# Kernel tuning notes

Measured on AMD Instinct MI355X. Metric: run time of the kernel, lower is better.

The kernel has to match this reference:

```python
import jax, jax.numpy as jnp
import numpy as np

D_MODEL = 640
KW = 32                                  # kernel_width -> content_kernel (compression (1,1))
SUPER = np.array([5, 5, 2, 1, 1])        # supersampling per subhead
DIL = np.array([1, 1, 2, 4, 8])          # dilation rate per subhead
SUBHEADS = 5
HEADS = int(SUPER.sum())                 # 14
DH = D_MODEL // SUBHEADS                 # 128
B, N = 2, 1024
KC = KW                                  # content kernel width
DIL_PER_HEAD = np.repeat(DIL, SUPER)     # dilation used by each of the 14 value heads


def _windows(seq, bias, dil):
    """Banded (dilated, stride-1, 'same'-padded) windows of a projected sequence.

    seq: (B, N, DH). The original zero-pads the raw sequence, then applies the
    per-head Linear; projecting a zero vector yields the bias, so padding the
    projected sequence with `bias` is mathematically identical.
    Returns (B, N, KC, DH) with out[b, l, j] = padded[b, l + j*dil].
    """
    dil = int(dil)
    pad_total = (KC - 1) * dil           # effective kernel minus 1, stride 1 -> same length
    pl = pad_total // 2
    pr = pad_total - pl
    b = seq.shape[0]
    left = jnp.broadcast_to(bias, (b, pl, DH))
    right = jnp.broadcast_to(bias, (b, pr, DH))
    padded = jnp.concatenate([left, seq, right], axis=1)
    idx = jnp.arange(N)[:, None] + jnp.arange(KC)[None, :] * dil  # (N, KC)
    return padded[:, idx]


def setup_inputs() -> dict:
    key = jax.random.key(0)
    ks = jax.random.split(key, 13)
    f = lambda k, sh, s=1.0: jax.random.normal(k, sh, dtype=jnp.float32) * s
    return {
        "query": f(ks[0], (B, N, D_MODEL)),
        "key": f(ks[1], (B, N, D_MODEL)),
        "value": f(ks[2], (B, N, D_MODEL)),
        "Qk": f(ks[3], (SUBHEADS, DH, D_MODEL), 0.04),
        "Qb": f(ks[4], (SUBHEADS, DH), 0.02),
        "Kk": f(ks[5], (SUBHEADS, DH, D_MODEL), 0.04),
        "Kb": f(ks[6], (SUBHEADS, DH), 0.02),
        "Vk": f(ks[7], (HEADS, DH, D_MODEL), 0.04),
        "Vb": f(ks[8], (HEADS, DH), 0.02),
        "Sk": f(ks[9], (HEADS, KC, KC), 0.1),   # Pos_Sampling kernel, Kq=1 so in=out=KC
        "Sb": f(ks[10], (HEADS, KC), 0.02),
        "Ck": f(ks[11], (D_MODEL, HEADS * DH), 0.02),  # Collapse kernel
        "Cb": f(ks[12], (D_MODEL,), 0.0),
    }


def reference(query, key, value, Qk, Qb, Kk, Kb, Vk, Vb, Sk, Sb, Ck, Cb):
    # Per-subhead Q/K projections (query_kernel=1, stride=1 -> one query per position)
    q = jnp.einsum('bnd,sod->bnso', query, Qk) + Qb          # (B,N,5,DH)
    kproj = jnp.einsum('bnd,sod->bnso', key, Kk) + Kb        # (B,N,5,DH)
    kwin = jnp.stack(
        [_windows(kproj[:, :, s], Kb[s], DIL[s]) for s in range(SUBHEADS)],
        axis=2)                                              # (B,N,5,KC,DH)
    # Banded scores (original applies no 1/sqrt(d) scaling)
    score = jnp.einsum('bnsd,bnskd->bnsk', q, kwin)          # (B,N,5,KC)
    # Supersample subhead scores into heads, then learned positional resampling
    score = jnp.repeat(score, SUPER, axis=2, total_repeat_length=HEADS)  # (B,N,14,KC)
    score = jnp.einsum('bnhk,hjk->bnhj', score, Sk) + Sb     # Pos_Sampling Linear
    w = jax.nn.softmax(score, axis=-1)
    # Per-head value projection; each head windows with its subhead's dilation
    vproj = jnp.einsum('bnd,hod->bnho', value, Vk) + Vb      # (B,N,14,DH)
    vwin = jnp.stack(
        [_windows(vproj[:, :, h], Vb[h], DIL_PER_HEAD[h]) for h in range(HEADS)],
        axis=2)                                              # (B,N,14,KC,DH)
    attn = jnp.einsum('bnhk,bnhkd->bnhd', w, vwin)           # (B,N,14,DH)
    flat = attn.reshape(attn.shape[0], attn.shape[1], HEADS * DH)
    return jnp.einsum('bnf,of->bno', flat, Ck) + Cb          # (B,N,D_MODEL)
```

## Files before the change

kernel.cpp:

```cpp
#include <hip/hip_runtime.h>
#include <hip/hip_bf16.h>

using bf16 = __hip_bfloat16;
typedef __attribute__((ext_vector_type(8))) short s16x8;
typedef __attribute__((ext_vector_type(4))) short s16x4;
typedef __attribute__((ext_vector_type(4))) float f32x4;
typedef unsigned int u32;

__device__ __forceinline__ float b2f(short u) {
    union { float f; u32 i; } x; x.i = ((u32)(unsigned short)u) << 16; return x.f;
}
__device__ __forceinline__ short f2b(float f) {
    bf16 h = (bf16)f; return *(short*)&h;
}

__device__ __forceinline__ void g2l16(const void* g, void* l) {
    __builtin_amdgcn_global_load_lds(
        (const __attribute__((address_space(1))) void*)g,
        (__attribute__((address_space(3))) void*)l, 16, 0, 0);
}

struct CvtArgs { const float* src[10]; bf16* dst[10]; int n[10]; int bb[11]; };
__global__ __launch_bounds__(256)
void convert_kernel(CvtArgs a) {
    const int blk = blockIdx.x;
    int s = 0;
    while (s < 9 && blk >= a.bb[s + 1]) ++s;
    const int base = (blk - a.bb[s]) * 1024 + threadIdx.x * 4;
    if (base >= a.n[s]) return;
    float4 v = *(const float4*)(a.src[s] + base);
    ushort4 o;
    o.x = (unsigned short)f2b(v.x); o.y = (unsigned short)f2b(v.y);
    o.z = (unsigned short)f2b(v.z); o.w = (unsigned short)f2b(v.w);
    *(ushort4*)(a.dst[s] + base) = o;
}

template<int BM, int BN, bool A_F32, bool OUT_F32>
__device__ __forceinline__ void gemm_pipe(
    const void* __restrict__ A, const bf16* __restrict__ W,
    const bf16* __restrict__ bias, void* __restrict__ out,
    int m0, int n0, int N, int K, bf16* lA, bf16* lB) {
    constexpr int WM = BM / 2, WN = BN / 2, FM = WM / 16, FN = WN / 16;
    constexpr int SA = BM / 64;
    constexpr int CA = BM / 64;
    constexpr int CB = BN / 64;
    constexpr int ASZ = BM * 32, BSZ = BN * 32;
    const int tid = threadIdx.x;
    const int wave = tid >> 6;
    const int lane = tid & 63;
    const int wr = wave >> 1, wc = wave & 1;
    const int quad = lane >> 4, lm = lane & 15;
    uint4 ra[SA];

    auto issueB = [&](int k0, int buf) {
#pragma unroll
        for (int c = 0; c < CB; ++c) {
            const int sl = c * 256 + tid, row = sl >> 2, col = (sl & 3) * 8;
            g2l16(W + (size_t)(n0 + row) * K + k0 + col,
                  lB + buf * BSZ + (c * 256 + wave * 64) * 8);
        }
    };
    auto issueA = [&](int k0, int buf) {
#pragma unroll
        for (int c = 0; c < CA; ++c) {
            const int sl = c * 256 + tid, row = sl >> 2, col = (sl & 3) * 8;
            g2l16((const bf16*)A + (size_t)(m0 + row) * K + k0 + col,
                  lA + buf * ASZ + (c * 256 + wave * 64) * 8);
        }
    };
    auto loadA_f32 = [&](int k0) {
#pragma unroll
        for (int q = 0; q < SA; ++q) {
            const int sl = q * 256 + tid, row = sl >> 2, col = (sl & 3) * 8;
            const float* g = (const float*)A + (size_t)(m0 + row) * K + k0 + col;
            float4 f0 = *(const float4*)g;
            float4 f1 = *(const float4*)(g + 4);
            union { uint4 u; short h[8]; } p;
            p.h[0] = f2b(f0.x); p.h[1] = f2b(f0.y); p.h[2] = f2b(f0.z); p.h[3] = f2b(f0.w);
            p.h[4] = f2b(f1.x); p.h[5] = f2b(f1.y); p.h[6] = f2b(f1.z); p.h[7] = f2b(f1.w);
            ra[q] = p.u;
        }
    };
    auto writeA = [&](int buf) {
#pragma unroll
        for (int q = 0; q < SA; ++q)
            *(uint4*)(lA + buf * ASZ + (q * 256 + tid) * 8) = ra[q];
    };

    f32x4 acc[FM][FN] = {};
    issueB(0, 0);
    if (A_F32) { loadA_f32(0); writeA(0); } else { issueA(0, 0); }
    __syncthreads();

    int cur = 0;
    for (int k0 = 0; k0 < K; k0 += 32) {
        const bool more = (k0 + 32 < K);
        if (more) {
            issueB(k0 + 32, cur ^ 1);
            if (A_F32) loadA_f32(k0 + 32); else issueA(k0 + 32, cur ^ 1);
        }
        s16x8 af[FM], bf_[FN];
#pragma unroll
        for (int i = 0; i < FM; ++i)
            af[i] = *(const s16x8*)&lA[cur * ASZ + (wr * WM + i * 16 + lm) * 32 + quad * 8];
#pragma unroll
        for (int j = 0; j < FN; ++j)
            bf_[j] = *(const s16x8*)&lB[cur * BSZ + (wc * WN + j * 16 + lm) * 32 + quad * 8];
#pragma unroll
        for (int i = 0; i < FM; ++i)
#pragma unroll
            for (int j = 0; j < FN; ++j)
                acc[i][j] = __builtin_amdgcn_mfma_f32_16x16x32_bf16(af[i], bf_[j], acc[i][j], 0, 0, 0);
        if (more && A_F32) writeA(cur ^ 1);
        __syncthreads();
        cur ^= 1;
    }
#pragma unroll
    for (int i = 0; i < FM; ++i) {
        const int rbase = m0 + wr * WM + i * 16 + quad * 4;
#pragma unroll
        for (int j = 0; j < FN; ++j) {
            const int col = n0 + wc * WN + j * 16 + lm;
            const float bv = (float)bias[col];
#pragma unroll
            for (int r = 0; r < 4; ++r) {
                float v = acc[i][j][r] + bv;
                size_t off = (size_t)(rbase + r) * N + col;
                if (OUT_F32) ((float*)out)[off] = v;
                else         ((bf16*)out)[off] = (bf16)v;
            }
        }
    }
}

__global__ __launch_bounds__(256)
void proj_kernel(const float* __restrict__ q, const float* __restrict__ k,
                 const float* __restrict__ v,
                 const bf16* __restrict__ Qkc, const bf16* __restrict__ Kkc,
                 const bf16* __restrict__ Vkc,
                 const bf16* __restrict__ Qbc, const bf16* __restrict__ Kbc,
                 const bf16* __restrict__ Vbc,
                 bf16* __restrict__ qp, bf16* __restrict__ kp,
                 bf16* __restrict__ vp) {
    __shared__ __align__(16) bf16 lA[2 * 128 * 32];
    __shared__ __align__(16) bf16 lB[2 * 64 * 32];
    const int L = blockIdx.x, xcd = L & 7, i = L >> 3;
    const int m0 = (xcd * 2 + i / 48) * 128;
    const int nid = i % 48;
    if (nid < 10)
        gemm_pipe<128, 64, true, false>(q, Qkc, Qbc, qp, m0, nid * 64, 640, 640, lA, lB);
    else if (nid < 20)
        gemm_pipe<128, 64, true, false>(k, Kkc, Kbc, kp, m0, (nid - 10) * 64, 640, 640, lA, lB);
    else
        gemm_pipe<128, 64, true, false>(v, Vkc, Vbc, vp, m0, (nid - 20) * 64, 1792, 640, lA, lB);
}

__global__ __launch_bounds__(256)
void collapse_kernel(const bf16* __restrict__ atn, const bf16* __restrict__ Ckc,
                     const bf16* __restrict__ Cbc, float* __restrict__ out) {
    __shared__ __align__(16) bf16 lA[2 * 64 * 32];
    __shared__ __align__(16) bf16 lB[2 * 64 * 32];
    const int L = blockIdx.x, xcd = L & 7, i = L >> 3;
    const int m0 = (xcd * 4 + i / 10) * 64;
    const int n0 = (i % 10) * 64;
    gemm_pipe<64, 64, false, true>(atn, Ckc, Cbc, out, m0, n0, 640, 1792, lA, lB);
}

__global__ __launch_bounds__(256)
void attn_v6(const bf16* __restrict__ qp, const bf16* __restrict__ kp,
             const bf16* __restrict__ vp,
             const bf16* __restrict__ Kbc, const bf16* __restrict__ Vbc,
             const bf16* __restrict__ Skc, const bf16* __restrict__ Sbc,
             bf16* __restrict__ atn) {
    const int pos = ((blockIdx.x & 7) << 8) | (blockIdx.x >> 3);
    const int b = pos >> 10, l = pos & 1023;
    const int t = threadIdx.x;
    __shared__ float qs[640];
    __shared__ float sc5[5 * 32];
    __shared__ float sc14[14 * 32];
    __shared__ float w14T[32 * 14];

    if (t < 80) {
        s16x8 qv = *(const s16x8*)((const short*)qp + (size_t)pos * 640 + t * 8);
#pragma unroll
        for (int r = 0; r < 8; ++r) qs[t * 8 + r] = b2f(qv[r]);
    }
    __syncthreads();

    {
        const int j = t >> 3, p = t & 7;
#pragma unroll
        for (int s = 0; s < 5; ++s) {
            const int dil = (s < 2) ? 1 : (1 << (s - 1));
            const int pl = (31 * dil) >> 1;
            const int row = l + j * dil - pl;
            const float* q = qs + s * 128 + p * 8;
            const short* kr = (row >= 0 && row < 1024)
                ? (const short*)kp + (size_t)((b << 10) | row) * 640 + s * 128 + p * 8
                : (const short*)Kbc + s * 128 + p * 8;
            float acc = 0.f;
#pragma unroll
            for (int g = 0; g < 2; ++g) {
                s16x8 kv = *(const s16x8*)(kr + g * 64);
                float4 q0 = *(const float4*)(q + g * 64);
                float4 q1 = *(const float4*)(q + g * 64 + 4);
                acc += q0.x * b2f(kv[0]) + q0.y * b2f(kv[1])
                     + q0.z * b2f(kv[2]) + q0.w * b2f(kv[3])
                     + q1.x * b2f(kv[4]) + q1.y * b2f(kv[5])
                     + q1.z * b2f(kv[6]) + q1.w * b2f(kv[7]);
            }
            acc += __shfl_xor(acc, 1);
            acc += __shfl_xor(acc, 2);
            acc += __shfl_xor(acc, 4);
            if (p == 0) sc5[s * 32 + j] = acc;
        }
    }
    __syncthreads();

    for (int idx = t; idx < 448; idx += 256) {
        const int h = idx >> 5;
        const int s = (h < 5) ? 0 : (h < 10) ? 1 : (h < 12) ? 2 : (h == 12) ? 3 : 4;
        const s16x8* sk = (const s16x8*)((const short*)Skc + idx * 32);
        const float* sc = sc5 + s * 32;
        float acc = b2f(((const short*)Sbc)[idx]);
#pragma unroll
        for (int g = 0; g < 4; ++g) {
            s16x8 kk = sk[g];
#pragma unroll
            for (int r = 0; r < 8; ++r) acc += sc[g * 8 + r] * b2f(kk[r]);
        }
        sc14[idx] = acc;
    }
    __syncthreads();

    if (t < 224) {
        const int h = t >> 4, u = t & 15;
        float s0 = sc14[h * 32 + u], s1 = sc14[h * 32 + u + 16];
        float mx = fmaxf(s0, s1);
#pragma unroll
        for (int m = 1; m < 16; m <<= 1) mx = fmaxf(mx, __shfl_xor(mx, m));
        float e0 = __expf(s0 - mx), e1 = __expf(s1 - mx);
        float sum = e0 + e1;
#pragma unroll
        for (int m = 1; m < 16; m <<= 1) sum += __shfl_xor(sum, m);
        float inv = 1.f / sum;
        w14T[u * 14 + h] = e0 * inv;
        w14T[(u + 16) * 14 + h] = e1 * inv;
    }
    __syncthreads();

    if (t < 224) {
        const int h = t >> 4, d8 = (t & 15) * 8;
        const int dil = (h < 10) ? 1 : (h < 12) ? 2 : (h == 12) ? 4 : 8;
        const int pl = (31 * dil) >> 1;
        const int col = h * 128 + d8;
        float acc[8] = {};
#pragma unroll
        for (int j = 0; j < 32; ++j) {
            const int row = l + j * dil - pl;
            const short* src = (row >= 0 && row < 1024)
                ? (const short*)vp + (size_t)((b << 10) | row) * 1792 + col
                : (const short*)Vbc + col;
            s16x8 v8 = *(const s16x8*)src;
            const float w = w14T[j * 14 + h];
#pragma unroll
            for (int r = 0; r < 8; ++r) acc[r] += w * b2f(v8[r]);
        }
        union { uint4 u; short h16[8]; } o;
#pragma unroll
        for (int r = 0; r < 8; ++r) o.h16[r] = f2b(acc[r]);
        *(uint4*)((short*)atn + (size_t)pos * 1792 + col) = o.u;
    }
}

extern "C" void kernel_launch(void* const* d_in, const int* in_sizes, int n_in,
                              void* d_out, int out_size, void* d_ws, size_t ws_size,
                              hipStream_t stream) {
    const int M = 2048;
    char* w = (char*)d_ws;
    size_t off = 0;
    auto alloc = [&](size_t bytes) -> char* {
        off = (off + 255) & ~(size_t)255;
        char* p = w + off; off += bytes; return p;
    };
    bf16* Qkc = (bf16*)alloc(409600 * 2);
    bf16* Qbc = (bf16*)alloc(640 * 2);
    bf16* Kkc = (bf16*)alloc(409600 * 2);
    bf16* Kbc = (bf16*)alloc(640 * 2);
    bf16* Vkc = (bf16*)alloc(1146880 * 2);
    bf16* Vbc = (bf16*)alloc(1792 * 2);
    bf16* Skc = (bf16*)alloc(14336 * 2);
    bf16* Sbc = (bf16*)alloc(448 * 2);
    bf16* Ckc = (bf16*)alloc(1146880 * 2);
    bf16* Cbc = (bf16*)alloc(640 * 2);
    bf16* qp = (bf16*)alloc((size_t)M * 640 * 2);
    bf16* kp = (bf16*)alloc((size_t)M * 640 * 2);
    bf16* vp = (bf16*)alloc((size_t)M * 1792 * 2);
    bf16* atn = (bf16*)alloc((size_t)M * 1792 * 2);

    CvtArgs ca;
    bf16* dsts[10] = {Qkc, Qbc, Kkc, Kbc, Vkc, Vbc, Skc, Sbc, Ckc, Cbc};
    const int ns[10] = {409600, 640, 409600, 640, 1146880, 1792, 14336, 448, 1146880, 640};
    int cum = 0;
    for (int i = 0; i < 10; ++i) {
        ca.src[i] = (const float*)d_in[3 + i];
        ca.dst[i] = dsts[i];
        ca.n[i] = ns[i];
        ca.bb[i] = cum;
        cum += (ns[i] + 1023) / 1024;
    }
    ca.bb[10] = cum;

    dim3 blk(256);
    convert_kernel<<<dim3(cum), blk, 0, stream>>>(ca);
    proj_kernel<<<dim3(768), blk, 0, stream>>>(
        (const float*)d_in[0], (const float*)d_in[1], (const float*)d_in[2],
        Qkc, Kkc, Vkc, Qbc, Kbc, Vbc, qp, kp, vp);
    attn_v6<<<dim3(2048), blk, 0, stream>>>(qp, kp, vp, Kbc, Vbc, Skc, Sbc, atn);
    collapse_kernel<<<dim3(320), blk, 0, stream>>>(atn, Ckc, Cbc, (float*)d_out);
}
```

Measured before the change: 167.0 us.

## Pre-convert activations to bf16 and triple-buffer GEMM LDS pipeline

Activations q/k/v are now converted to bf16 in the shared convert kernel, so the projection GEMM can load both operands with direct global-to-LDS transfers instead of loading fp32 into registers and converting. The GEMM helper becomes a three-stage LDS ring with two tiles in flight, using explicit vmcnt waits and raw barriers in place of __syncthreads. The attention kernel also gains a fast path for interior positions that skips the per-row bounds check and padding selection. The cost is an extra bf16 activation round trip through memory, more LDS per block, and reliance on hand-tuned waitcnt values being correct.

```diff
diff --git a/kernel.cpp b/kernel.cpp
--- a/kernel.cpp
+++ b/kernel.cpp
@@ -20,12 +20,12 @@
         (__attribute__((address_space(3))) void*)l, 16, 0, 0);
 }
 
-struct CvtArgs { const float* src[10]; bf16* dst[10]; int n[10]; int bb[11]; };
+struct CvtArgs { const float* src[13]; bf16* dst[13]; int n[13]; int bb[14]; };
 __global__ __launch_bounds__(256)
 void convert_kernel(CvtArgs a) {
     const int blk = blockIdx.x;
     int s = 0;
-    while (s < 9 && blk >= a.bb[s + 1]) ++s;
+    while (s < 12 && blk >= a.bb[s + 1]) ++s;
     const int base = (blk - a.bb[s]) * 1024 + threadIdx.x * 4;
     if (base >= a.n[s]) return;
     float4 v = *(const float4*)(a.src[s] + base);
@@ -35,24 +35,27 @@
     *(ushort4*)(a.dst[s] + base) = o;
 }
 
-template<int BM, int BN, bool A_F32, bool OUT_F32>
-__device__ __forceinline__ void gemm_pipe(
-    const void* __restrict__ A, const bf16* __restrict__ W,
+template<int BM, int BN, bool OUT_F32>
+__device__ __forceinline__ void gemm3(
+    const bf16* __restrict__ A, const bf16* __restrict__ W,
     const bf16* __restrict__ bias, void* __restrict__ out,
     int m0, int n0, int N, int K, bf16* lA, bf16* lB) {
     constexpr int WM = BM / 2, WN = BN / 2, FM = WM / 16, FN = WN / 16;
-    constexpr int SA = BM / 64;
-    constexpr int CA = BM / 64;
-    constexpr int CB = BN / 64;
+    constexpr int CA = BM / 64, CB = BN / 64;
     constexpr int ASZ = BM * 32, BSZ = BN * 32;
+    constexpr int NV = CA + CB;
     const int tid = threadIdx.x;
-    const int wave = tid >> 6;
-    const int lane = tid & 63;
+    const int wave = tid >> 6, lane = tid & 63;
     const int wr = wave >> 1, wc = wave & 1;
     const int quad = lane >> 4, lm = lane & 15;
-    uint4 ra[SA];
-
-    auto issueB = [&](int k0, int buf) {
+
+    auto issue = [&](int k0, int buf) {
+#pragma unroll
+        for (int c = 0; c < CA; ++c) {
+            const int sl = c * 256 + tid, row = sl >> 2, col = (sl & 3) * 8;
+            g2l16(A + (size_t)(m0 + row) * K + k0 + col,
+                  lA + buf * ASZ + (c * 256 + wave * 64) * 8);
+        }
 #pragma unroll
         for (int c = 0; c < CB; ++c) {
             const int sl = c * 256 + tid, row = sl >> 2, col = (sl & 3) * 8;
@@ -60,60 +63,50 @@
                   lB + buf * BSZ + (c * 256 + wave * 64) * 8);
         }
     };
-    auto issueA = [&](int k0, int buf) {
-#pragma unroll
-        for (int c = 0; c < CA; ++c) {
-            const int sl = c * 256 + tid, row = sl >> 2, col = (sl & 3) * 8;
-            g2l16((const bf16*)A + (size_t)(m0 + row) * K + k0 + col,
-                  lA + buf * ASZ + (c * 256 + wave * 64) * 8);
-        }
-    };
-    auto loadA_f32 = [&](int k0) {
-#pragma unroll
-        for (int q = 0; q < SA; ++q) {
-            const int sl = q * 256 + tid, row = sl >> 2, col = (sl & 3) * 8;
-            const float* g = (const float*)A + (size_t)(m0 + row) * K + k0 + col;
-            float4 f0 = *(const float4*)g;
-            float4 f1 = *(const float4*)(g + 4);
-            union { uint4 u; short h[8]; } p;
-            p.h[0] = f2b(f0.x); p.h[1] = f2b(f0.y); p.h[2] = f2b(f0.z); p.h[3] = f2b(f0.w);
-            p.h[4] = f2b(f1.x); p.h[5] = f2b(f1.y); p.h[6] = f2b(f1.z); p.h[7] = f2b(f1.w);
-            ra[q] = p.u;
-        }
-    };
-    auto writeA = [&](int buf) {
-#pragma unroll
-        for (int q = 0; q < SA; ++q)
-            *(uint4*)(lA + buf * ASZ + (q * 256 + tid) * 8) = ra[q];
-    };
-
+
+    const int ns = K / 32;
     f32x4 acc[FM][FN] = {};
-    issueB(0, 0);
-    if (A_F32) { loadA_f32(0); writeA(0); } else { issueA(0, 0); }
-    __syncthreads();
+
+    issue(0, 0); issue(32, 1);
+    if constexpr (NV == 2) asm volatile("s_waitcnt vmcnt(2)" ::: "memory");
+    else                   asm volatile("s_waitcnt vmcnt(3)" ::: "memory");
+    __builtin_amdgcn_sched_barrier(0);
+    __builtin_amdgcn_s_barrier();
+    __builtin_amdgcn_sched_barrier(0);
 
     int cur = 0;
-    for (int k0 = 0; k0 < K; k0 += 32) {
-        const bool more = (k0 + 32 < K);
-        if (more) {
-            issueB(k0 + 32, cur ^ 1);
-            if (A_F32) loadA_f32(k0 + 32); else issueA(k0 + 32, cur ^ 1);
-        }
+    for (int k = 0; k < ns; ++k) {
+        if (k + 2 < ns) {
+            int b2 = cur + 2; if (b2 >= 3) b2 -= 3;
+            issue((k + 2) * 32, b2);
+        }
+        const bf16* cA = lA + cur * ASZ;
+        const bf16* cB = lB + cur * BSZ;
         s16x8 af[FM], bf_[FN];
 #pragma unroll
         for (int i = 0; i < FM; ++i)
-            af[i] = *(const s16x8*)&lA[cur * ASZ + (wr * WM + i * 16 + lm) * 32 + quad * 8];
+            af[i] = *(const s16x8*)&cA[(wr * WM + i * 16 + lm) * 32 + quad * 8];
 #pragma unroll
         for (int j = 0; j < FN; ++j)
-            bf_[j] = *(const s16x8*)&lB[cur * BSZ + (wc * WN + j * 16 + lm) * 32 + quad * 8];
+            bf_[j] = *(const s16x8*)&cB[(wc * WN + j * 16 + lm) * 32 + quad * 8];
 #pragma unroll
         for (int i = 0; i < FM; ++i)
 #pragma unroll
             for (int j = 0; j < FN; ++j)
                 acc[i][j] = __builtin_amdgcn_mfma_f32_16x16x32_bf16(af[i], bf_[j], acc[i][j], 0, 0, 0);
-        if (more && A_F32) writeA(cur ^ 1);
-        __syncthreads();
-        cur ^= 1;
+        if (k + 2 < ns) {
+            if constexpr (NV == 2) asm volatile("s_waitcnt vmcnt(2) lgkmcnt(0)" ::: "memory");
+            else                   asm volatile("s_waitcnt vmcnt(3) lgkmcnt(0)" ::: "memory");
+            __builtin_amdgcn_sched_barrier(0);
+            __builtin_amdgcn_s_barrier();
+            __builtin_amdgcn_sched_barrier(0);
+        } else if (k + 1 < ns) {
+            asm volatile("s_waitcnt vmcnt(0) lgkmcnt(0)" ::: "memory");
+            __builtin_amdgcn_sched_barrier(0);
+            __builtin_amdgcn_s_barrier();
+            __builtin_amdgcn_sched_barrier(0);
+        }
+        cur += 1; if (cur >= 3) cur = 0;
     }
 #pragma unroll
     for (int i = 0; i < FM; ++i) {
@@ -134,36 +127,36 @@
 }
 
 __global__ __launch_bounds__(256)
-void proj_kernel(const float* __restrict__ q, const float* __restrict__ k,
-                 const float* __restrict__ v,
+void proj_kernel(const bf16* __restrict__ qb, const bf16* __restrict__ kb,
+                 const bf16* __restrict__ vb,
                  const bf16* __restrict__ Qkc, const bf16* __restrict__ Kkc,
                  const bf16* __restrict__ Vkc,
                  const bf16* __restrict__ Qbc, const bf16* __restrict__ Kbc,
                  const bf16* __restrict__ Vbc,
                  bf16* __restrict__ qp, bf16* __restrict__ kp,
                  bf16* __restrict__ vp) {
-    __shared__ __align__(16) bf16 lA[2 * 128 * 32];
-    __shared__ __align__(16) bf16 lB[2 * 64 * 32];
+    __shared__ __align__(16) bf16 lA[3 * 128 * 32];
+    __shared__ __align__(16) bf16 lB[3 * 64 * 32];
     const int L = blockIdx.x, xcd = L & 7, i = L >> 3;
     const int m0 = (xcd * 2 + i / 48) * 128;
     const int nid = i % 48;
     if (nid < 10)
-        gemm_pipe<128, 64, true, false>(q, Qkc, Qbc, qp, m0, nid * 64, 640, 640, lA, lB);
+        gemm3<128, 64, false>(qb, Qkc, Qbc, qp, m0, nid * 64, 640, 640, lA, lB);
     else if (nid < 20)
-        gemm_pipe<128, 64, true, false>(k, Kkc, Kbc, kp, m0, (nid - 10) * 64, 640, 640, lA, lB);
+        gemm3<128, 64, false>(kb, Kkc, Kbc, kp, m0, (nid - 10) * 64, 640, 640, lA, lB);
     else
-        gemm_pipe<128, 64, true, false>(v, Vkc, Vbc, vp, m0, (nid - 20) * 64, 1792, 640, lA, lB);
+        gemm3<128, 64, false>(vb, Vkc, Vbc, vp, m0, (nid - 20) * 64, 1792, 640, lA, lB);
 }
 
 __global__ __launch_bounds__(256)
 void collapse_kernel(const bf16* __restrict__ atn, const bf16* __restrict__ Ckc,
                      const bf16* __restrict__ Cbc, float* __restrict__ out) {
-    __shared__ __align__(16) bf16 lA[2 * 64 * 32];
-    __shared__ __align__(16) bf16 lB[2 * 64 * 32];
+    __shared__ __align__(16) bf16 lA[3 * 64 * 32];
+    __shared__ __align__(16) bf16 lB[3 * 64 * 32];
     const int L = blockIdx.x, xcd = L & 7, i = L >> 3;
     const int m0 = (xcd * 4 + i / 10) * 64;
     const int n0 = (i % 10) * 64;
-    gemm_pipe<64, 64, false, true>(atn, Ckc, Cbc, out, m0, n0, 640, 1792, lA, lB);
+    gemm3<64, 64, true>(atn, Ckc, Cbc, out, m0, n0, 640, 1792, lA, lB);
 }
 
 __global__ __launch_bounds__(256)
@@ -193,21 +186,32 @@
         for (int s = 0; s < 5; ++s) {
             const int dil = (s < 2) ? 1 : (1 << (s - 1));
             const int pl = (31 * dil) >> 1;
-            const int row = l + j * dil - pl;
             const float* q = qs + s * 128 + p * 8;
-            const short* kr = (row >= 0 && row < 1024)
-                ? (const short*)kp + (size_t)((b << 10) | row) * 640 + s * 128 + p * 8
-                : (const short*)Kbc + s * 128 + p * 8;
-            float acc = 0.f;
-#pragma unroll
-            for (int g = 0; g < 2; ++g) {
-                s16x8 kv = *(const s16x8*)(kr + g * 64);
-                float4 q0 = *(const float4*)(q + g * 64);
-                float4 q1 = *(const float4*)(q + g * 64 + 4);
-                acc += q0.x * b2f(kv[0]) + q0.y * b2f(kv[1])
-                     + q0.z * b2f(kv[2]) + q0.w * b2f(kv[3])
-                     + q1.x * b2f(kv[4]) + q1.y * b2f(kv[5])
-                     + q1.z * b2f(kv[6]) + q1.w * b2f(kv[7]);
+            auto dot = [&](const short* kr) -> float {
+                float a = 0.f;
+#pragma unroll
+                for (int g = 0; g < 2; ++g) {
+                    s16x8 kv = *(const s16x8*)(kr + g * 64);
+                    float4 q0 = *(const float4*)(q + g * 64);
+                    float4 q1 = *(const float4*)(q + g * 64 + 4);
+                    a += q0.x * b2f(kv[0]) + q0.y * b2f(kv[1])
+                       + q0.z * b2f(kv[2]) + q0.w * b2f(kv[3])
+                       + q1.x * b2f(kv[4]) + q1.y * b2f(kv[5])
+                       + q1.z * b2f(kv[6]) + q1.w * b2f(kv[7]);
+                }
+                return a;
+            };
+            float acc;
+            if (l - pl >= 0 && l + 31 * dil - pl < 1024) {
+                const short* kr = (const short*)kp
+                    + (size_t)((b << 10) + l - pl + j * dil) * 640 + s * 128 + p * 8;
+                acc = dot(kr);
+            } else {
+                const int row = l + j * dil - pl;
+                const short* kr = (row >= 0 && row < 1024)
+                    ? (const short*)kp + (size_t)((b << 10) | row) * 640 + s * 128 + p * 8
+                    : (const short*)Kbc + s * 128 + p * 8;
+                acc = dot(kr);
             }
             acc += __shfl_xor(acc, 1);
             acc += __shfl_xor(acc, 2);
@@ -255,16 +259,29 @@
         const int pl = (31 * dil) >> 1;
         const int col = h * 128 + d8;
         float acc[8] = {};
-#pragma unroll
-        for (int j = 0; j < 32; ++j) {
-            const int row = l + j * dil - pl;
-            const short* src = (row >= 0 && row < 1024)
-                ? (const short*)vp + (size_t)((b << 10) | row) * 1792 + col
-                : (const short*)Vbc + col;
-            s16x8 v8 = *(const s16x8*)src;
-            const float w = w14T[j * 14 + h];
-#pragma unroll
-            for (int r = 0; r < 8; ++r) acc[r] += w * b2f(v8[r]);
+        if (l - pl >= 0 && l + 31 * dil - pl < 1024) {
+            const short* src = (const short*)vp
+                + (size_t)((b << 10) + l - pl) * 1792 + col;
+            const size_t stride = (size_t)dil * 1792;
+#pragma unroll
+            for (int j = 0; j < 32; ++j) {
+                s16x8 v8 = *(const s16x8*)(src + j * stride);
+                const float w = w14T[j * 14 + h];
+#pragma unroll
+                for (int r = 0; r < 8; ++r) acc[r] += w * b2f(v8[r]);
+            }
+        } else {
+#pragma unroll
+            for (int j = 0; j < 32; ++j) {
+                const int row = l + j * dil - pl;
+                const short* src = (row >= 0 && row < 1024)
+                    ? (const short*)vp + (size_t)((b << 10) | row) * 1792 + col
+                    : (const short*)Vbc + col;
+                s16x8 v8 = *(const s16x8*)src;
+                const float w = w14T[j * 14 + h];
+#pragma unroll
+                for (int r = 0; r < 8; ++r) acc[r] += w * b2f(v8[r]);
+            }
         }
         union { uint4 u; short h16[8]; } o;
 #pragma unroll
@@ -293,29 +310,32 @@
     bf16* Sbc = (bf16*)alloc(448 * 2);
     bf16* Ckc = (bf16*)alloc(1146880 * 2);
     bf16* Cbc = (bf16*)alloc(640 * 2);
-    bf16* qp = (bf16*)alloc((size_t)M * 640 * 2);
-    bf16* kp = (bf16*)alloc((size_t)M * 640 * 2);
-    bf16* vp = (bf16*)alloc((size_t)M * 1792 * 2);
+    bf16* qb  = (bf16*)alloc((size_t)M * 640 * 2);
+    bf16* kb  = (bf16*)alloc((size_t)M * 640 * 2);
+    bf16* vb  = (bf16*)alloc((size_t)M * 640 * 2);
+    bf16* qp  = (bf16*)alloc((size_t)M * 640 * 2);
+    bf16* kp  = (bf16*)alloc((size_t)M * 640 * 2);
+    bf16* vp  = (bf16*)alloc((size_t)M * 1792 * 2);
     bf16* atn = (bf16*)alloc((size_t)M * 1792 * 2);
 
     CvtArgs ca;
-    bf16* dsts[10] = {Qkc, Qbc, Kkc, Kbc, Vkc, Vbc, Skc, Sbc, Ckc, Cbc};
-    const int ns[10] = {409600, 640, 409600, 640, 1146880, 1792, 14336, 448, 1146880, 640};
+    bf16* dsts[13] = {Qkc, Qbc, Kkc, Kbc, Vkc, Vbc, Skc, Sbc, Ckc, Cbc, qb, kb, vb};
+    const int ns[13] = {409600, 640, 409600, 640, 1146880, 1792, 14336, 448,
+                        1146880, 640, 1310720, 1310720, 1310720};
     int cum = 0;
-    for (int i = 0; i < 10; ++i) {
-        ca.src[i] = (const float*)d_in[3 + i];
+    for (int i = 0; i < 13; ++i) {
+        ca.src[i] = (const float*)d_in[i < 10 ? 3 + i : i - 10];
         ca.dst[i] = dsts[i];
         ca.n[i] = ns[i];
         ca.bb[i] = cum;
         cum += (ns[i] + 1023) / 1024;
     }
-    ca.bb[10] = cum;
+    ca.bb[13] = cum;
 
     dim3 blk(256);
     convert_kernel<<<dim3(cum), blk, 0, stream>>>(ca);
     proj_kernel<<<dim3(768), blk, 0, stream>>>(
-        (const float*)d_in[0], (const float*)d_in[1], (const float*)d_in[2],
-        Qkc, Kkc, Vkc, Qbc, Kbc, Vbc, qp, kp, vp);
+        qb, kb, vb, Qkc, Kkc, Vkc, Qbc, Kbc, Vbc, qp, kp, vp);
     attn_v6<<<dim3(2048), blk, 0, stream>>>(qp, kp, vp, Kbc, Vbc, Skc, Sbc, atn);
     collapse_kernel<<<dim3(320), blk, 0, stream>>>(atn, Ckc, Cbc, (float*)d_out);
 }
```

Result: no change. 167.6 us (+0.4%).
